# Performance work log

Measured on AMD Instinct MI355X. Metric: run time of the kernel, lower is better.

## Reference

```python
import jax, jax.numpy as jnp
import numpy as np

N_NODES = 100000
N_EDGES = 3200000
IN_CH = 256
OUT_CH = 10


def setup_inputs() -> dict:
    key = jax.random.key(0)
    k1, k2, k3, k4 = jax.random.split(key, 4)
    x = jax.random.normal(k1, (N_NODES, IN_CH), dtype=jnp.float32)
    edge_index = jax.random.randint(k2, (2, N_EDGES), 0, N_NODES, dtype=jnp.int64)
    W_mu = jax.random.normal(k3, (IN_CH, OUT_CH), dtype=jnp.float32) * (1.0 / np.sqrt(IN_CH))
    b_mu = jnp.zeros((OUT_CH,), dtype=jnp.float32)
    W_logstd = jax.random.normal(k4, (IN_CH, OUT_CH), dtype=jnp.float32) * (1.0 / np.sqrt(IN_CH))
    b_logstd = jnp.zeros((OUT_CH,), dtype=jnp.float32)
    return {"x": x, "edge_index": edge_index, "W_mu": W_mu, "b_mu": b_mu,
            "W_logstd": W_logstd, "b_logstd": b_logstd}


def _gcn_norm(edge_index, num_nodes):
    # PyG gcn_norm: add self loops, deg from target (col), norm = d^-1/2[row]*d^-1/2[col]
    loop = jnp.arange(num_nodes, dtype=edge_index.dtype)
    row = jnp.concatenate([edge_index[0], loop])  # source nodes
    col = jnp.concatenate([edge_index[1], loop])  # target nodes
    deg = jax.ops.segment_sum(jnp.ones_like(col, dtype=jnp.float32), col,
                              num_segments=num_nodes)
    dinv = jax.lax.rsqrt(jnp.maximum(deg, 1.0))  # self loops guarantee deg>=1
    norm = dinv[row] * dinv[col]  # [E+N]
    return row, col, norm


def _gcn_conv(x, W, b, row, col, norm, num_nodes):
    h = x @ W                               # [N, out]  linear transform first
    msg = h[row] * norm[:, None]            # gather + scale, [E+N, out]
    out = jax.ops.segment_sum(msg, col, num_segments=num_nodes)  # scatter-add
    return out + b


def reference(x, edge_index, W_mu, b_mu, W_logstd, b_logstd):
    n = x.shape[0]
    row, col, norm = _gcn_norm(edge_index, n)
    mu = _gcn_conv(x, W_mu, b_mu, row, col, norm, n)
    logstd = _gcn_conv(x, W_logstd, b_logstd, row, col, norm, n)
    return mu, logstd
```

## Files before the change

kernel.cpp:

```cpp
#include <hip/hip_runtime.h>
#include <math.h>

#define N_NODES 100000
#define N_EDGES 3200000
#define IN_CH 256
#define NC 20
#define OC 10
#define NPB 128
#define NBUCK 782
#define CAP 4864
#define CHUNK 4096
#define NCHUNK 782

__global__ __launch_bounds__(256) void k_initptr(int* __restrict__ bptr) {
    int i = blockIdx.x * 256 + threadIdx.x;
    if (i < NBUCK) bptr[i] = i * CAP;
}

__global__ __launch_bounds__(256) void k_bin2v(const int* __restrict__ row,
                                               const int* __restrict__ col,
                                               int* __restrict__ bptr,
                                               int* __restrict__ bpairs) {
    __shared__ int lh[NBUCK];
    __shared__ int lbase[NBUCK];
    int t = threadIdx.x;
    int e0 = blockIdx.x * CHUNK;
    int nE = N_EDGES - e0; if (nE > CHUNK) nE = CHUNK;
    int n4 = nE >> 2;
    const int4* c4 = (const int4*)(col + e0);
    const int4* r4 = (const int4*)(row + e0);

    for (int i = t; i < NBUCK; i += 256) lh[i] = 0;
    __syncthreads();
    for (int j = t; j < n4; j += 256) {
        int4 c = c4[j];
        atomicAdd(&lh[c.x >> 7], 1); atomicAdd(&lh[c.y >> 7], 1);
        atomicAdd(&lh[c.z >> 7], 1); atomicAdd(&lh[c.w >> 7], 1);
    }
    __syncthreads();
    for (int i = t; i < NBUCK; i += 256) {
        int c = lh[i];
        lbase[i] = c ? atomicAdd(&bptr[i], c) : 0;
        lh[i] = 0;
    }
    __syncthreads();
    for (int j = t; j < n4; j += 256) {
        int4 c = c4[j];
        int4 r = r4[j];
        int b0 = c.x >> 7, b1 = c.y >> 7, b2 = c.z >> 7, b3 = c.w >> 7;
        int q0 = atomicAdd(&lh[b0], 1);
        int q1 = atomicAdd(&lh[b1], 1);
        int q2 = atomicAdd(&lh[b2], 1);
        int q3 = atomicAdd(&lh[b3], 1);
        int s0 = lbase[b0] + q0, s1 = lbase[b1] + q1;
        int s2 = lbase[b2] + q2, s3 = lbase[b3] + q3;
        if (s0 < (b0 + 1) * CAP) bpairs[s0] = (r.x << 7) | (c.x & 127);
        if (s1 < (b1 + 1) * CAP) bpairs[s1] = (r.y << 7) | (c.y & 127);
        if (s2 < (b2 + 1) * CAP) bpairs[s2] = (r.z << 7) | (c.z & 127);
        if (s3 < (b3 + 1) * CAP) bpairs[s3] = (r.w << 7) | (c.w & 127);
    }
}

__global__ __launch_bounds__(256) void k_deg(const int* __restrict__ bptr,
                                             const int* __restrict__ bpairs,
                                             float* __restrict__ dinv) {
    __shared__ int lc[NPB];
    int b = blockIdx.x, t = threadIdx.x;
    if (t < NPB) lc[t] = 0;
    __syncthreads();
    int start = b * CAP;
    int n = bptr[b] - start; if (n > CAP) n = CAP;
    for (int p = t; p < n; p += 256)
        atomicAdd(&lc[bpairs[start + p] & 127], 1);
    __syncthreads();
    int node = b * NPB + t;
    if (t < NPB && node < N_NODES)
        dinv[node] = rsqrtf((float)(lc[t] + 1));
}

__device__ __forceinline__ unsigned bfpack(float a, float b) {
    unsigned ua = __float_as_uint(a), ub = __float_as_uint(b);
    ua = (ua + 0x7FFFu + ((ua >> 16) & 1u)) >> 16;
    ub = (ub + 0x7FFFu + ((ub >> 16) & 1u)) >> 16;
    return ua | (ub << 16);
}
__device__ __forceinline__ float bflo(unsigned p) { return __uint_as_float(p << 16); }
__device__ __forceinline__ float bfhi(unsigned p) { return __uint_as_float(p & 0xFFFF0000u); }

__global__ __launch_bounds__(256) void k_gemm2(const float* __restrict__ x,
                                               const float* __restrict__ Wmu,
                                               const float* __restrict__ Wls,
                                               const float* __restrict__ dinv,
                                               unsigned* __restrict__ hbf) {
    __shared__ float sW[NC * 272];
    int t = threadIdx.x;
    for (int idx = t; idx < IN_CH * OC; idx += 256) {
        int k = idx / OC, c = idx - k * OC;
        int kk = k >> 6, j = k & 63;
        sW[c * 272 + kk * 68 + j]          = Wmu[idx];
        sW[(c + OC) * 272 + kk * 68 + j]   = Wls[idx];
    }
    __syncthreads();

    int node = blockIdx.x * 64 + (t >> 2);
    int kk = t & 3;
    if (node >= N_NODES) return;

    const float4* x4 = (const float4*)(x + (size_t)node * IN_CH);
    float acc[NC];
#pragma unroll
    for (int c = 0; c < NC; c++) acc[c] = 0.0f;

#pragma unroll 4
    for (int j4 = 0; j4 < 16; j4++) {
        float4 xv = x4[kk * 16 + j4];
#pragma unroll
        for (int c = 0; c < NC; c++) {
            float4 w = *(const float4*)&sW[c * 272 + kk * 68 + j4 * 4];
            acc[c] += xv.x * w.x + xv.y * w.y + xv.z * w.z + xv.w * w.w;
        }
    }

#pragma unroll
    for (int c = 0; c < NC; c++) {
        acc[c] += __shfl_xor(acc[c], 2);
        acc[c] += __shfl_xor(acc[c], 1);
    }

    if (kk == 0) {
        float d = dinv[node];
        unsigned* hp = hbf + (size_t)node * 10;
        *(uint2*)(hp + 0) = make_uint2(bfpack(acc[0] * d,  acc[1] * d),
                                       bfpack(acc[2] * d,  acc[3] * d));
        *(uint2*)(hp + 2) = make_uint2(bfpack(acc[4] * d,  acc[5] * d),
                                       bfpack(acc[6] * d,  acc[7] * d));
        *(uint2*)(hp + 4) = make_uint2(bfpack(acc[8] * d,  acc[9] * d),
                                       bfpack(acc[10] * d, acc[11] * d));
        *(uint2*)(hp + 6) = make_uint2(bfpack(acc[12] * d, acc[13] * d),
                                       bfpack(acc[14] * d, acc[15] * d));
        *(uint2*)(hp + 8) = make_uint2(bfpack(acc[16] * d, acc[17] * d),
                                       bfpack(acc[18] * d, acc[19] * d));
    }
}

__global__ __launch_bounds__(256) void k_agg4(const int* __restrict__ bptr,
                                              const int* __restrict__ bpairs,
                                              const unsigned* __restrict__ hbf,
                                              const float* __restrict__ bmu,
                                              const float* __restrict__ bls,
                                              float* __restrict__ out) {
    __shared__ int lcnt[NPB];
    __shared__ int lscan[NPB];
    __shared__ int sCnt[NPB];
    __shared__ int ssrc[CAP];
    int b = blockIdx.x, t = threadIdx.x;
    int start = b * CAP;
    int n = bptr[b] - start; if (n > CAP) n = CAP;

    if (t < NPB) lcnt[t] = 0;
    __syncthreads();
    for (int p = t; p < n; p += 256)
        atomicAdd(&lcnt[bpairs[start + p] & 127], 1);
    __syncthreads();

    int cnt = 0;
    if (t < NPB) { cnt = lcnt[t]; lscan[t] = cnt; sCnt[t] = cnt; }
    __syncthreads();
    for (int o = 1; o < NPB; o <<= 1) {
        int add = 0;
        if (t < NPB && t >= o) add = lscan[t - o];
        __syncthreads();
        if (t < NPB) lscan[t] += add;
        __syncthreads();
    }
    if (t < NPB) lcnt[t] = lscan[t] - cnt;
    __syncthreads();

    for (int p = t; p < n; p += 256) {
        int pk = bpairs[start + p];
        int q = atomicAdd(&lcnt[pk & 127], 1);
        ssrc[q] = ((unsigned)pk) >> 7;
    }
    __syncthreads();

    int nl = t >> 1, half = t & 1;
    int node = b * NPB + nl;
    int ccnt = sCnt[nl];
    int base = lscan[nl] - ccnt;
    int mid = ccnt >> 1;
    int j0 = half ? mid : 0;
    int j1 = half ? ccnt : mid;

    float a[NC];
#pragma unroll
    for (int c = 0; c < NC; c++) a[c] = 0.0f;

#define ADDROW(R)                                                        \
    {                                                                    \
        const unsigned* hp_ = hbf + (size_t)(R) * 10;                    \
        uint2 q0 = *(const uint2*)(hp_ + 0);                             \
        uint2 q1 = *(const uint2*)(hp_ + 2);                             \
        uint2 q2 = *(const uint2*)(hp_ + 4);                             \
        uint2 q3 = *(const uint2*)(hp_ + 6);                             \
        uint2 q4 = *(const uint2*)(hp_ + 8);                             \
        a[0]  += bflo(q0.x); a[1]  += bfhi(q0.x);                        \
        a[2]  += bflo(q0.y); a[3]  += bfhi(q0.y);                        \
        a[4]  += bflo(q1.x); a[5]  += bfhi(q1.x);                        \
        a[6]  += bflo(q1.y); a[7]  += bfhi(q1.y);                        \
        a[8]  += bflo(q2.x); a[9]  += bfhi(q2.x);                        \
        a[10] += bflo(q2.y); a[11] += bfhi(q2.y);                        \
        a[12] += bflo(q3.x); a[13] += bfhi(q3.x);                        \
        a[14] += bflo(q3.y); a[15] += bfhi(q3.y);                        \
        a[16] += bflo(q4.x); a[17] += bfhi(q4.x);                        \
        a[18] += bflo(q4.y); a[19] += bfhi(q4.y);                        \
    }

    int j = j0;
    for (; j + 1 < j1; j += 2) {
        int r0 = ssrc[base + j];
        int r1 = ssrc[base + j + 1];
        ADDROW(r0);
        ADDROW(r1);
    }
    if (j < j1) {
        int r0 = ssrc[base + j];
        ADDROW(r0);
    }
    if (half == 0 && node < N_NODES) ADDROW(node);
#undef ADDROW

#pragma unroll
    for (int c = 0; c < NC; c++) a[c] += __shfl_xor(a[c], 1);

    if (half == 0 && node < N_NODES) {
        float dn = rsqrtf((float)(ccnt + 1));
        float* om = out + (size_t)node * OC;
        float* ol = out + (size_t)N_NODES * OC + (size_t)node * OC;
#pragma unroll
        for (int c = 0; c < OC; c++) {
            om[c] = dn * a[c]      + bmu[c];
            ol[c] = dn * a[c + OC] + bls[c];
        }
    }
}

__global__ __launch_bounds__(256) void k_init_deg(float* __restrict__ deg) {
    int i = blockIdx.x * 256 + threadIdx.x;
    if (i < N_NODES) deg[i] = 1.0f;
}
__global__ __launch_bounds__(256) void k_count(const int* __restrict__ col, float* __restrict__ deg) {
    int e = blockIdx.x * 256 + threadIdx.x;
    if (e < N_EDGES) atomicAdd(&deg[col[e]], 1.0f);
}
__global__ __launch_bounds__(256) void k_dinvk(float* __restrict__ deg) {
    int i = blockIdx.x * 256 + threadIdx.x;
    if (i < N_NODES) deg[i] = rsqrtf(deg[i]);
}
__global__ __launch_bounds__(256) void k_gemm_f32(const float* __restrict__ x,
                                                  const float* __restrict__ Wmu,
                                                  const float* __restrict__ Wls,
                                                  float* __restrict__ h) {
    int node = blockIdx.x * 256 + threadIdx.x;
    if (node >= N_NODES) return;
    const float4* x4 = (const float4*)(x + (size_t)node * IN_CH);
    float acc[NC];
#pragma unroll
    for (int c = 0; c < NC; c++) acc[c] = 0.0f;
    for (int k4 = 0; k4 < IN_CH / 4; k4++) {
        float4 xv = x4[k4];
        float xk[4] = {xv.x, xv.y, xv.z, xv.w};
#pragma unroll
        for (int kk = 0; kk < 4; kk++) {
            const float* wm = Wmu + (k4 * 4 + kk) * OC;
            const float* wl = Wls + (k4 * 4 + kk) * OC;
#pragma unroll
            for (int c = 0; c < OC; c++) {
                acc[c]      += xk[kk] * wm[c];
                acc[c + OC] += xk[kk] * wl[c];
            }
        }
    }
    float* hp = h + (size_t)node * NC;
#pragma unroll
    for (int c = 0; c < NC; c++) hp[c] = acc[c];
}
__global__ __launch_bounds__(256) void k_scatter(const int* __restrict__ row, const int* __restrict__ col,
                                                 const float* __restrict__ dinv, const float* __restrict__ h,
                                                 float* __restrict__ out) {
    int e = blockIdx.x * 256 + threadIdx.x;
    if (e >= N_EDGES) return;
    int r = row[e], c = col[e];
    float s = dinv[r] * dinv[c];
    const float* hp = h + (size_t)r * NC;
    float* om = out + (size_t)c * OC;
    float* ol = om + (size_t)N_NODES * OC;
#pragma unroll
    for (int k = 0; k < OC; k++) atomicAdd(om + k, hp[k] * s);
#pragma unroll
    for (int k = 0; k < OC; k++) atomicAdd(ol + k, hp[OC + k] * s);
}
__global__ __launch_bounds__(256) void k_final(const float* __restrict__ h, const float* __restrict__ dinv,
                                               const float* __restrict__ bmu, const float* __restrict__ bls,
                                               float* __restrict__ out) {
    int i = blockIdx.x * 256 + threadIdx.x;
    if (i >= N_NODES * OC) return;
    int node = i / OC, c = i - node * OC;
    float d = dinv[node];
    float d2 = d * d;
    out[i]                += h[node * NC + c]      * d2 + bmu[c];
    out[N_NODES * OC + i] += h[node * NC + OC + c] * d2 + bls[c];
}

extern "C" void kernel_launch(void* const* d_in, const int* in_sizes, int n_in,
                              void* d_out, int out_size, void* d_ws, size_t ws_size,
                              hipStream_t stream) {
    const float* x   = (const float*)d_in[0];
    const int*   ei  = (const int*)d_in[1];
    const float* Wmu = (const float*)d_in[2];
    const float* bmu = (const float*)d_in[3];
    const float* Wls = (const float*)d_in[4];
    const float* bls = (const float*)d_in[5];
    float* out = (float*)d_out;

    const int* row = ei;
    const int* col = ei + N_EDGES;

    const size_t BPAIRS_OFF = (size_t)(9 << 19);
    const size_t REQ = BPAIRS_OFF + (size_t)NBUCK * CAP * 4;

    if (ws_size >= REQ) {
        char* w = (char*)d_ws;
        int*      bptr   = (int*)(w);
        float*    dinv   = (float*)(w + 8192);
        unsigned* hbf    = (unsigned*)(w + (512 << 10));
        int*      bpairs = (int*)(w + BPAIRS_OFF);

        k_initptr<<<(NBUCK + 255) / 256, 256, 0, stream>>>(bptr);
        k_bin2v<<<NCHUNK, 256, 0, stream>>>(row, col, bptr, bpairs);
        k_deg<<<NBUCK, 256, 0, stream>>>(bptr, bpairs, dinv);
        k_gemm2<<<(N_NODES + 63) / 64, 256, 0, stream>>>(x, Wmu, Wls, dinv, hbf);
        k_agg4<<<NBUCK, 256, 0, stream>>>(bptr, bpairs, hbf, bmu, bls, out);
    } else {
        float* deg = (float*)d_ws;
        float* h   = (float*)((char*)d_ws + (1 << 20));
        hipMemsetAsync(d_out, 0, (size_t)out_size * sizeof(float), stream);
        k_init_deg<<<(N_NODES + 255) / 256, 256, 0, stream>>>(deg);
        k_count<<<(N_EDGES + 255) / 256, 256, 0, stream>>>(col, deg);
        k_dinvk<<<(N_NODES + 255) / 256, 256, 0, stream>>>(deg);
        k_gemm_f32<<<(N_NODES + 255) / 256, 256, 0, stream>>>(x, Wmu, Wls, h);
        k_scatter<<<(N_EDGES + 255) / 256, 256, 0, stream>>>(row, col, deg, h, out);
        k_final<<<(N_NODES * OC + 255) / 256, 256, 0, stream>>>(h, deg, bmu, bls, out);
    }
}
```

Before: 309.1 us.

## Stage binned edges in LDS for coalesced writes; process four nodes per GEMM thread

The binning kernel now uses 1024-thread blocks over 8192-edge chunks. It computes a local prefix scan of bucket counts, sorts edges into a shared staging buffer, then writes them to global bucket slots in contiguous runs instead of scattered single-word stores. The GEMM kernel has each thread handle four nodes so every shared-memory weight load is reused four times, at the cost of 80 accumulators per thread. The scan adds several barriers and fewer blocks run, and register pressure in the GEMM may reduce occupancy.

```diff
diff --git a/kernel.cpp b/kernel.cpp
--- a/kernel.cpp
+++ b/kernel.cpp
@@ -9,55 +9,79 @@
 #define NPB 128
 #define NBUCK 782
 #define CAP 4864
-#define CHUNK 4096
-#define NCHUNK 782
+
+#define CHUNK3 8192
+#define NCHUNK3 391
 
 __global__ __launch_bounds__(256) void k_initptr(int* __restrict__ bptr) {
     int i = blockIdx.x * 256 + threadIdx.x;
     if (i < NBUCK) bptr[i] = i * CAP;
 }
 
-__global__ __launch_bounds__(256) void k_bin2v(const int* __restrict__ row,
+__global__ __launch_bounds__(1024) void k_bin3(const int* __restrict__ row,
                                                const int* __restrict__ col,
                                                int* __restrict__ bptr,
                                                int* __restrict__ bpairs) {
-    __shared__ int lh[NBUCK];
-    __shared__ int lbase[NBUCK];
+    __shared__ int   lh[NBUCK];
+    __shared__ int   lscan[NBUCK];
+    __shared__ int   gmino[NBUCK];
+    __shared__ int   stage[CHUNK3];
+    __shared__ unsigned short sbkt[CHUNK3];
+
     int t = threadIdx.x;
-    int e0 = blockIdx.x * CHUNK;
-    int nE = N_EDGES - e0; if (nE > CHUNK) nE = CHUNK;
+    int e0 = blockIdx.x * CHUNK3;
+    int nE = N_EDGES - e0; if (nE > CHUNK3) nE = CHUNK3;
     int n4 = nE >> 2;
     const int4* c4 = (const int4*)(col + e0);
     const int4* r4 = (const int4*)(row + e0);
 
-    for (int i = t; i < NBUCK; i += 256) lh[i] = 0;
-    __syncthreads();
-    for (int j = t; j < n4; j += 256) {
+    for (int i = t; i < NBUCK; i += 1024) lh[i] = 0;
+    __syncthreads();
+
+    for (int j = t; j < n4; j += 1024) {
         int4 c = c4[j];
         atomicAdd(&lh[c.x >> 7], 1); atomicAdd(&lh[c.y >> 7], 1);
         atomicAdd(&lh[c.z >> 7], 1); atomicAdd(&lh[c.w >> 7], 1);
     }
     __syncthreads();
-    for (int i = t; i < NBUCK; i += 256) {
-        int c = lh[i];
-        lbase[i] = c ? atomicAdd(&bptr[i], c) : 0;
-        lh[i] = 0;
-    }
-    __syncthreads();
-    for (int j = t; j < n4; j += 256) {
+
+    int cnt = 0;
+    if (t < NBUCK) { cnt = lh[t]; lscan[t] = cnt; }
+    __syncthreads();
+    for (int o = 1; o < NBUCK; o <<= 1) {
+        int add = 0;
+        if (t < NBUCK && t >= o) add = lscan[t - o];
+        __syncthreads();
+        if (t < NBUCK) lscan[t] += add;
+        __syncthreads();
+    }
+    if (t < NBUCK) {
+        int lofs = lscan[t] - cnt;
+        int gbase = cnt ? atomicAdd(&bptr[t], cnt) : 0;
+        gmino[t] = gbase - lofs;
+        lh[t] = lofs;
+    }
+    __syncthreads();
+
+    for (int j = t; j < n4; j += 1024) {
         int4 c = c4[j];
         int4 r = r4[j];
         int b0 = c.x >> 7, b1 = c.y >> 7, b2 = c.z >> 7, b3 = c.w >> 7;
-        int q0 = atomicAdd(&lh[b0], 1);
-        int q1 = atomicAdd(&lh[b1], 1);
-        int q2 = atomicAdd(&lh[b2], 1);
-        int q3 = atomicAdd(&lh[b3], 1);
-        int s0 = lbase[b0] + q0, s1 = lbase[b1] + q1;
-        int s2 = lbase[b2] + q2, s3 = lbase[b3] + q3;
-        if (s0 < (b0 + 1) * CAP) bpairs[s0] = (r.x << 7) | (c.x & 127);
-        if (s1 < (b1 + 1) * CAP) bpairs[s1] = (r.y << 7) | (c.y & 127);
-        if (s2 < (b2 + 1) * CAP) bpairs[s2] = (r.z << 7) | (c.z & 127);
-        if (s3 < (b3 + 1) * CAP) bpairs[s3] = (r.w << 7) | (c.w & 127);
+        int s0 = atomicAdd(&lh[b0], 1);
+        int s1 = atomicAdd(&lh[b1], 1);
+        int s2 = atomicAdd(&lh[b2], 1);
+        int s3 = atomicAdd(&lh[b3], 1);
+        stage[s0] = (r.x << 7) | (c.x & 127); sbkt[s0] = (unsigned short)b0;
+        stage[s1] = (r.y << 7) | (c.y & 127); sbkt[s1] = (unsigned short)b1;
+        stage[s2] = (r.z << 7) | (c.z & 127); sbkt[s2] = (unsigned short)b2;
+        stage[s3] = (r.w << 7) | (c.w & 127); sbkt[s3] = (unsigned short)b3;
+    }
+    __syncthreads();
+
+    for (int j = t; j < nE; j += 1024) {
+        int b = sbkt[j];
+        int dst = gmino[b] + j;
+        if (dst < (b + 1) * CAP) bpairs[dst] = stage[j];
     }
 }
 
@@ -87,7 +111,7 @@
 __device__ __forceinline__ float bflo(unsigned p) { return __uint_as_float(p << 16); }
 __device__ __forceinline__ float bfhi(unsigned p) { return __uint_as_float(p & 0xFFFF0000u); }
 
-__global__ __launch_bounds__(256) void k_gemm2(const float* __restrict__ x,
+__global__ __launch_bounds__(256) void k_gemm3(const float* __restrict__ x,
                                                const float* __restrict__ Wmu,
                                                const float* __restrict__ Wls,
                                                const float* __restrict__ dinv,
@@ -102,44 +126,67 @@
     }
     __syncthreads();
 
-    int node = blockIdx.x * 64 + (t >> 2);
     int kk = t & 3;
-    if (node >= N_NODES) return;
-
-    const float4* x4 = (const float4*)(x + (size_t)node * IN_CH);
-    float acc[NC];
-#pragma unroll
-    for (int c = 0; c < NC; c++) acc[c] = 0.0f;
+    int slot = t >> 2;
+    int n0 = blockIdx.x * 256 + slot;
+
+    int nd[4];
+#pragma unroll
+    for (int u = 0; u < 4; u++) {
+        int n = n0 + u * 64;
+        nd[u] = (n < N_NODES) ? n : (N_NODES - 1);
+    }
+
+    float acc[4][NC];
+#pragma unroll
+    for (int u = 0; u < 4; u++)
+#pragma unroll
+        for (int c = 0; c < NC; c++) acc[u][c] = 0.0f;
+
+    const float4* x4 = (const float4*)x;
 
 #pragma unroll 4
     for (int j4 = 0; j4 < 16; j4++) {
-        float4 xv = x4[kk * 16 + j4];
+        float4 xv0 = x4[(size_t)nd[0] * 64 + kk * 16 + j4];
+        float4 xv1 = x4[(size_t)nd[1] * 64 + kk * 16 + j4];
+        float4 xv2 = x4[(size_t)nd[2] * 64 + kk * 16 + j4];
+        float4 xv3 = x4[(size_t)nd[3] * 64 + kk * 16 + j4];
 #pragma unroll
         for (int c = 0; c < NC; c++) {
             float4 w = *(const float4*)&sW[c * 272 + kk * 68 + j4 * 4];
-            acc[c] += xv.x * w.x + xv.y * w.y + xv.z * w.z + xv.w * w.w;
+            acc[0][c] += xv0.x * w.x + xv0.y * w.y + xv0.z * w.z + xv0.w * w.w;
+            acc[1][c] += xv1.x * w.x + xv1.y * w.y + xv1.z * w.z + xv1.w * w.w;
+            acc[2][c] += xv2.x * w.x + xv2.y * w.y + xv2.z * w.z + xv2.w * w.w;
+            acc[3][c] += xv3.x * w.x + xv3.y * w.y + xv3.z * w.z + xv3.w * w.w;
         }
     }
 
 #pragma unroll
-    for (int c = 0; c < NC; c++) {
-        acc[c] += __shfl_xor(acc[c], 2);
-        acc[c] += __shfl_xor(acc[c], 1);
-    }
+    for (int u = 0; u < 4; u++)
+#pragma unroll
+        for (int c = 0; c < NC; c++) {
+            acc[u][c] += __shfl_xor(acc[u][c], 2);
+            acc[u][c] += __shfl_xor(acc[u][c], 1);
+        }
 
     if (kk == 0) {
-        float d = dinv[node];
-        unsigned* hp = hbf + (size_t)node * 10;
-        *(uint2*)(hp + 0) = make_uint2(bfpack(acc[0] * d,  acc[1] * d),
-                                       bfpack(acc[2] * d,  acc[3] * d));
-        *(uint2*)(hp + 2) = make_uint2(bfpack(acc[4] * d,  acc[5] * d),
-                                       bfpack(acc[6] * d,  acc[7] * d));
-        *(uint2*)(hp + 4) = make_uint2(bfpack(acc[8] * d,  acc[9] * d),
-                                       bfpack(acc[10] * d, acc[11] * d));
-        *(uint2*)(hp + 6) = make_uint2(bfpack(acc[12] * d, acc[13] * d),
-                                       bfpack(acc[14] * d, acc[15] * d));
-        *(uint2*)(hp + 8) = make_uint2(bfpack(acc[16] * d, acc[17] * d),
-                                       bfpack(acc[18] * d, acc[19] * d));
+#pragma unroll
+        for (int u = 0; u < 4; u++) {
+            int n = n0 + u * 64;
+            if (n >= N_NODES) continue;
+            float d = dinv[n];
+            unsigned* hp = hbf + (size_t)n * 10;
+            *(uint2*)(hp + 0) = make_uint2(bfpack(acc[u][0] * d,  acc[u][1] * d),
+                                           bfpack(acc[u][2] * d,  acc[u][3] * d));
+            *(uint2*)(hp + 2) = make_uint2(bfpack(acc[u][4] * d,  acc[u][5] * d),
+                                           bfpack(acc[u][6] * d,  acc[u][7] * d));
+            *(uint2*)(hp + 4) = make_uint2(bfpack(acc[u][8] * d,  acc[u][9] * d),
+                                           bfpack(acc[u][10] * d, acc[u][11] * d));
+            *(uint2*)(hp + 6) = make_uint2(bfpack(acc[u][12] * d, acc[u][13] * d),
+                                           bfpack(acc[u][14] * d, acc[u][15] * d));
+            *(uint2*)(hp + 8) = make_uint2(bfpack(acc[u][16] * d, acc[u][17] * d),
+                                           bfpack(acc[u][18] * d, acc[u][19] * d));
+        }
     }
 }
 
@@ -336,9 +383,9 @@
         int*      bpairs = (int*)(w + BPAIRS_OFF);
 
         k_initptr<<<(NBUCK + 255) / 256, 256, 0, stream>>>(bptr);
-        k_bin2v<<<NCHUNK, 256, 0, stream>>>(row, col, bptr, bpairs);
+        k_bin3<<<NCHUNK3, 1024, 0, stream>>>(row, col, bptr, bpairs);
         k_deg<<<NBUCK, 256, 0, stream>>>(bptr, bpairs, dinv);
-        k_gemm2<<<(N_NODES + 63) / 64, 256, 0, stream>>>(x, Wmu, Wls, dinv, hbf);
+        k_gemm3<<<(N_NODES + 255) / 256, 256, 0, stream>>>(x, Wmu, Wls, dinv, hbf);
         k_agg4<<<NBUCK, 256, 0, stream>>>(bptr, bpairs, hbf, bmu, bls, out);
     } else {
         float* deg = (float*)d_ws;
```

Result: faster. 265.6 us (-14.1%).
